# Optimization experiments

Measured on AMD Instinct MI355X. Metric: run time of the kernel, lower is better.

The kernel has to match this reference:

```python
import jax, jax.numpy as jnp
import numpy as np

B, S, D, H = 64, 256, 2048, 16
HD = D // H  # 128
MAXS = 256


def setup_inputs() -> dict:
    key = jax.random.key(0)
    ks = jax.random.split(key, 16)
    sc = 0.02
    inp = {
        "q": jax.random.normal(ks[0], (B, S, D), jnp.float32),
        "k": jax.random.normal(ks[1], (B, S, D), jnp.float32),
        "v": jax.random.normal(ks[2], (B, S, D), jnp.float32),
        "attention_mask": jax.random.randint(ks[3], (B, S), 0, 2, jnp.int32),
        # projection weights, torch Linear convention: y = x @ W.T + b
        "Wq": jax.random.normal(ks[4], (D, D), jnp.float32) * sc,
        "bq": jnp.zeros((D,), jnp.float32),
        "Wk": jax.random.normal(ks[5], (D, D), jnp.float32) * sc,
        "bk": jnp.zeros((D,), jnp.float32),
        "Wv": jax.random.normal(ks[6], (D, D), jnp.float32) * sc,
        "bv": jnp.zeros((D,), jnp.float32),
        "Wo": jax.random.normal(ks[7], (D, D), jnp.float32) * sc,
        "bo": jnp.zeros((D,), jnp.float32),
        # additive per-head bias table (max_sequence_length=256)
        "bias_table": jax.random.normal(ks[8], (H, MAXS, MAXS), jnp.float32) * 0.1,
    }
    return inp


def reference(q, k, v, attention_mask, Wq, bq, Wk, bk, Wv, bv, Wo, bo, bias_table):
    def proj(x, W, b):  # (B,S,D) -> (B,H,S,HD)
        y = x @ W.T + b
        return y.reshape(B, S, H, HD).transpose(0, 2, 1, 3)

    qh = proj(q, Wq, bq)
    kh = proj(k, Wk, bk)
    vh = proj(v, Wv, bv)

    # (B,H,Sq,Sk) scores
    scores = jnp.einsum("bhqd,bhkd->bhqk", qh, kh) / jnp.sqrt(jnp.float32(HD))
    scores = scores + bias_table[None, :, :S, :S]
    # mask: (B,Sk) -> (B,1,1,Sk); masked_fill where mask==0
    neg_inf = jnp.finfo(scores.dtype).min
    scores = jnp.where(attention_mask[:, None, None, :] == 0, neg_inf, scores)
    probs = jax.nn.softmax(scores, axis=-1)  # dropout p=0.0 -> identity
    out = jnp.einsum("bhqk,bhkd->bhqd", probs, vh)
    out = out.transpose(0, 2, 1, 3).reshape(B, S, D)
    return out @ Wo.T + bo
```

## Files before the change

### kernel.cpp

```cpp
#include <hip/hip_runtime.h>
#include <hip/hip_bf16.h>

typedef __attribute__((ext_vector_type(4))) float f32x4;
typedef __attribute__((ext_vector_type(8))) short s16x8;
typedef __attribute__((ext_vector_type(4))) unsigned short u16x4;
typedef __attribute__((ext_vector_type(8))) unsigned short u16x8;
typedef __attribute__((ext_vector_type(4))) int i32x4;

#define NB 64
#define NS 256
#define ND 2048
#define NH 16
#define NHD 128

__device__ __forceinline__ unsigned short f2bf(float f){
  unsigned int u = __float_as_uint(f);
  u += 0x7fffu + ((u >> 16) & 1u);
  return (unsigned short)(u >> 16);
}

__device__ __forceinline__ void gload16(const void* g, void* l){
  __builtin_amdgcn_global_load_lds(
    (const __attribute__((address_space(1))) unsigned int*)g,
    (__attribute__((address_space(3))) unsigned int*)l, 16, 0, 0);
}

#define SBAR()  __builtin_amdgcn_sched_barrier(0)
#define BARRIER() do{ SBAR(); __builtin_amdgcn_s_barrier(); SBAR(); }while(0)
#define WAIT_LGKM0() do{ asm volatile("s_waitcnt lgkmcnt(0)" ::: "memory"); SBAR(); }while(0)
#define WAIT_VM0()   do{ asm volatile("s_waitcnt vmcnt(0)"   ::: "memory"); SBAR(); }while(0)
#define WAIT_VM8()   do{ asm volatile("s_waitcnt vmcnt(8)"   ::: "memory"); SBAR(); }while(0)

__global__ __launch_bounds__(256) void wconv(const float* __restrict__ s,
                                             unsigned short* __restrict__ d, int n8){
  int i = blockIdx.x*256 + threadIdx.x;
  if (i >= n8) return;
  f32x4 a = *(const f32x4*)(s + (size_t)i*8);
  f32x4 b = *(const f32x4*)(s + (size_t)i*8 + 4);
  u16x8 u;
  #pragma unroll
  for (int r=0;r<4;r++){ u[r]=f2bf(a[r]); u[4+r]=f2bf(b[r]); }
  *(u16x8*)(d + (size_t)i*8) = u;
}

template<int OUTMODE>
__global__ __launch_bounds__(512, 2) void gemm256(
    const unsigned short* __restrict__ A, const unsigned short* __restrict__ Bw,
    const float* __restrict__ bias, void* __restrict__ Out, int m_base)
{
  extern __shared__ __attribute__((aligned(16))) char ldsb[];
  const int tid  = threadIdx.x;
  const int lane = tid & 63, wid = tid >> 6;
  const int g = lane >> 4, l15 = lane & 15;
  const int wm = wid >> 2, wn = wid & 3;

  const int nwg = gridDim.x, bid = blockIdx.x;
  const int swz = (bid & 7) * (nwg >> 3) + (bid >> 3);
  const int mt = swz >> 3, nt = swz & 7;
  const int m0 = mt*256, n0 = nt*256;

  const int srow_l = tid >> 3;
  const int scol   = (((tid & 7) ^ (srow_l & 7)) * 8);
  const unsigned short* gsrc[4];
  gsrc[0] = A  + (size_t)(m0 +       srow_l)*ND + scol;
  gsrc[1] = A  + (size_t)(m0 + 128 + srow_l)*ND + scol;
  gsrc[2] = Bw + (size_t)(n0 +       srow_l)*ND + scol;
  gsrc[3] = Bw + (size_t)(n0 + 128 + srow_l)*ND + scol;

#define STAGE(buf, p, kt) do{ \
    const unsigned short* s_ = gsrc[p] + (kt); \
    char* d_ = ldsb + (buf)*65536 + ((p)>>1)*32768 + ((p)&1)*16384 + tid*16; \
    gload16(s_, d_); gload16(s_ + (size_t)64*ND, d_ + 8192); }while(0)

#define RD_A(buf, qa) do{ \
    _Pragma("unroll") for (int i_=0;i_<4;i_++){ \
      int hr = (qa)*64 + i_*16 + l15; \
      const char* p_ = ldsb + (buf)*65536 + wm*16384 + hr*128; \
      _Pragma("unroll") for (int ks_=0;ks_<2;ks_++) \
        av[i_][ks_] = *(const s16x8*)(p_ + (((ks_*4+g) ^ (hr&7))*16)); } }while(0)

#define RD_B(buf, dst, qb) do{ \
    _Pragma("unroll") for (int j_=0;j_<2;j_++){ \
      int hc = (wn&1)*64 + (qb)*32 + j_*16 + l15; \
      const char* p_ = ldsb + (buf)*65536 + 32768 + (wn>>1)*16384 + hc*128; \
      _Pragma("unroll") for (int ks_=0;ks_<2;ks_++) \
        dst[j_][ks_] = *(const s16x8*)(p_ + (((ks_*4+g) ^ (hc&7))*16)); } }while(0)

#define MFMA_PH(qa, qb, bv) do{ \
    __builtin_amdgcn_s_setprio(1); \
    _Pragma("unroll") for (int i_=0;i_<4;i_++) \
      _Pragma("unroll") for (int j_=0;j_<2;j_++) \
        _Pragma("unroll") for (int ks_=0;ks_<2;ks_++) \
          acc[(qa)*4+i_][(qb)*2+j_] = __builtin_amdgcn_mfma_f32_16x16x32_bf16( \
              av[i_][ks_], bv[j_][ks_], acc[(qa)*4+i_][(qb)*2+j_], 0,0,0); \
    __builtin_amdgcn_s_setprio(0); }while(0)

  f32x4 acc[8][4];
  s16x8 av[4][2], bva[2][2], bvb[2][2];

  STAGE(0,0,0); STAGE(0,1,0); STAGE(0,2,0); STAGE(0,3,0);
  #pragma unroll
  for (int i=0;i<8;i++)
    #pragma unroll
    for (int j=0;j<4;j++) acc[i][j] = f32x4{0.f,0.f,0.f,0.f};
  WAIT_VM0();
  BARRIER();

  for (int t = 0; t < 16; ++t) {
    const int kt1 = t*128 + 64, kt2 = t*128 + 128;
    RD_A(0,0); RD_B(0,bva,0);
    STAGE(1,0,kt1); STAGE(1,1,kt1); STAGE(1,2,kt1); STAGE(1,3,kt1);
    BARRIER(); WAIT_LGKM0();
    MFMA_PH(0,0,bva);
    BARRIER();
    RD_B(0,bvb,1);
    BARRIER(); WAIT_LGKM0();
    MFMA_PH(0,1,bvb);
    BARRIER();
    RD_A(0,1);
    BARRIER(); WAIT_LGKM0();
    MFMA_PH(1,0,bva);
    MFMA_PH(1,1,bvb);
    WAIT_VM0();
    BARRIER();
    RD_A(1,0); RD_B(1,bva,0);
    if (t < 15){ STAGE(0,0,kt2); STAGE(0,1,kt2); STAGE(0,2,kt2); STAGE(0,3,kt2); }
    BARRIER(); WAIT_LGKM0();
    MFMA_PH(0,0,bva);
    BARRIER();
    RD_B(1,bvb,1);
    BARRIER(); WAIT_LGKM0();
    MFMA_PH(0,1,bvb);
    BARRIER();
    RD_A(1,1);
    BARRIER(); WAIT_LGKM0();
    MFMA_PH(1,0,bva);
    MFMA_PH(1,1,bvb);
    WAIT_VM0();
    BARRIER();
  }

  #pragma unroll
  for (int jx=0;jx<4;jx++){
    int n = n0 + wn*64 + ((jx>>1)<<5) + ((jx&1)<<4) + l15;
    float bj = bias[n];
    #pragma unroll
    for (int i=0;i<8;i++){
      int mb = m_base + m0 + wm*128 + ((i>>2)<<6) + ((i&3)<<4) + g*4;
      if (OUTMODE == 2){
        float* O = (float*)Out;
        #pragma unroll
        for (int r=0;r<4;r++) O[(size_t)(mb+r)*ND + n] = acc[i][jx][r] + bj;
      } else if (OUTMODE == 0){
        unsigned short* O = (unsigned short*)Out;
        int bb = mb >> 8, h = n >> 7, d = n & 127, s0 = mb & 255;
        #pragma unroll
        for (int r=0;r<4;r++)
          O[(((size_t)bb*NH + h)*NS + s0 + r)*NHD + d] = f2bf(acc[i][jx][r] + bj);
      } else {
        unsigned short* O = (unsigned short*)Out;
        int bb = mb >> 8, h = n >> 7, d = n & 127, s0 = mb & 255;
        u16x4 u;
        #pragma unroll
        for (int r=0;r<4;r++) u[r] = f2bf(acc[i][jx][r] + bj);
        *(u16x4*)(O + (((size_t)bb*NH + h)*NHD + d)*NS + s0) = u;
      }
    }
  }
#undef STAGE
#undef RD_A
#undef RD_B
#undef MFMA_PH
}

__global__ __launch_bounds__(512, 1) void attn_fused2(
  const unsigned short* __restrict__ Qh, const unsigned short* __restrict__ Kh,
  const unsigned short* __restrict__ VT, const int* __restrict__ mask,
  const float* __restrict__ bias_table, unsigned short* __restrict__ AO)
{
  __shared__ unsigned short Klds[256*128];
  __shared__ unsigned short Vlds[128*256];
  char* Kb_ = (char*)Klds; char* Vb_ = (char*)Vlds;
  const int bh = blockIdx.x, b = bh >> 4, h = bh & 15;
  const int tid = threadIdx.x, lane = tid & 63, w = tid >> 6;
  const int g = lane >> 4, l15 = lane & 15;

  {
    const unsigned short* Ksrc = Kh + (size_t)bh*NS*NHD;
    int r0 = tid >> 4, sl = tid & 15;
    #pragma unroll
    for (int c=0;c<8;c++){
      int row = c*32 + r0;
      gload16(Ksrc + (size_t)row*NHD + ((sl ^ (row&7))*8), Kb_ + c*8192 + tid*16);
    }
  }
  {
    const unsigned short* Vsrc = VT + (size_t)bh*NHD*NS;
    int r0 = tid >> 5, sl = tid & 31;
    #pragma unroll
    for (int c=0;c<8;c++){
      int row = c*16 + r0;
      gload16(Vsrc + (size_t)row*NS + ((sl ^ (row&7))*8), Vb_ + c*8192 + tid*16);
    }
  }
  WAIT_VM8();
  BARRIER();

  const float scale = 0.08838834764831845f;
  const int* mrow = mask + b*NS;
  const int s0l = l15 + ((g&1)<<5), s1l = s0l + 16;
  const int sel = g >> 1;

  auto pass = [&](int p, bool wait_v){
    const int q = w*32 + p*16 + l15;
    const unsigned short* Qrow = Qh + ((size_t)bh*NS + q)*NHD;
    s16x8 bq[4];
    #pragma unroll
    for (int kk=0;kk<4;kk++) bq[kk] = *(const s16x8*)(Qrow + kk*32 + g*8);

    f32x4 c[16];
    __builtin_amdgcn_s_setprio(1);
    #pragma unroll
    for (int kb=0;kb<16;kb++){
      c[kb] = f32x4{0.f,0.f,0.f,0.f};
      int row = kb*16 + l15;
      #pragma unroll
      for (int kk=0;kk<4;kk++){
        s16x8 a = *(const s16x8*)(Kb_ + row*256 + (((kk*4+g) ^ (row&7))*16));
        c[kb] = __builtin_amdgcn_mfma_f32_16x16x32_bf16(a, bq[kk], c[kb], 0,0,0);
      }
    }
    __builtin_amdgcn_s_setprio(0);

    const float* brow = bias_table + ((size_t)h*NS + q)*NS;
    float mx = -3.0e38f;
    #pragma unroll
    for (int kb=0;kb<16;kb++){
      f32x4 b4 = *(const f32x4*)(brow + kb*16 + g*4);
      i32x4 m4 = *(const i32x4*)(mrow + kb*16 + g*4);
      #pragma unroll
      for (int r=0;r<4;r++){
        float val = (m4[r] != 0) ? (c[kb][r]*scale + b4[r]) : -3.0e38f;
        c[kb][r] = val;
        mx = fmaxf(mx, val);
      }
    }
    mx = fmaxf(mx, __shfl_xor(mx, 16));
    mx = fmaxf(mx, __shfl_xor(mx, 32));
    float sum = 0.f;
    #pragma unroll
    for (int kb=0;kb<16;kb++)
      #pragma unroll
      for (int r=0;r<4;r++){
        float pv = __expf(c[kb][r] - mx);
        c[kb][r] = pv; sum += pv;
      }
    sum += __shfl_xor(sum, 16);
    sum += __shfl_xor(sum, 32);
    float inv = 1.f / sum;

    unsigned int pk[16][2];
    #pragma unroll
    for (int kb=0;kb<16;kb++){
      pk[kb][0] = (unsigned int)f2bf(c[kb][0]*inv) | ((unsigned int)f2bf(c[kb][1]*inv) << 16);
      pk[kb][1] = (unsigned int)f2bf(c[kb][2]*inv) | ((unsigned int)f2bf(c[kb][3]*inv) << 16);
    }

    if (wait_v){ WAIT_VM0(); BARRIER(); }

    s16x8 pb[8];
    #pragma unroll
    for (int kk=0;kk<8;kk++){
      unsigned int e0 = (unsigned int)__shfl((int)pk[2*kk][0],   s0l);
      unsigned int e1 = (unsigned int)__shfl((int)pk[2*kk][1],   s0l);
      unsigned int e2 = (unsigned int)__shfl((int)pk[2*kk][0],   s1l);
      unsigned int e3 = (unsigned int)__shfl((int)pk[2*kk][1],   s1l);
      unsigned int o0 = (unsigned int)__shfl((int)pk[2*kk+1][0], s0l);
      unsigned int o1 = (unsigned int)__shfl((int)pk[2*kk+1][1], s0l);
      unsigned int o2 = (unsigned int)__shfl((int)pk[2*kk+1][0], s1l);
      unsigned int o3 = (unsigned int)__shfl((int)pk[2*kk+1][1], s1l);
      union { unsigned int wd[4]; s16x8 v; } u_;
      u_.wd[0] = sel ? o0 : e0; u_.wd[1] = sel ? o1 : e1;
      u_.wd[2] = sel ? o2 : e2; u_.wd[3] = sel ? o3 : e3;
      pb[kk] = u_.v;
    }

    f32x4 oacc[8];
    __builtin_amdgcn_s_setprio(1);
    #pragma unroll
    for (int dt=0;dt<8;dt++){
      oacc[dt] = f32x4{0.f,0.f,0.f,0.f};
      int row = dt*16 + l15;
      #pragma unroll
      for (int kk=0;kk<8;kk++){
        s16x8 a = *(const s16x8*)(Vb_ + row*512 + (((kk*4+g) ^ (row&7))*16));
        oacc[dt] = __builtin_amdgcn_mfma_f32_16x16x32_bf16(a, pb[kk], oacc[dt], 0,0,0);
      }
    }
    __builtin_amdgcn_s_setprio(0);

    #pragma unroll
    for (int dt=0;dt<8;dt++){
      u16x4 u;
      #pragma unroll
      for (int r=0;r<4;r++) u[r] = f2bf(oacc[dt][r]);
      *(u16x4*)(AO + ((size_t)b*NS + q)*ND + h*NHD + dt*16 + g*4) = u;
    }
  };

  pass(0, true);
  pass(1, false);
}

extern "C" void kernel_launch(void* const* d_in, const int* in_sizes, int n_in,
                              void* d_out, int out_size, void* d_ws, size_t ws_size,
                              hipStream_t stream)
{
  const float* q  = (const float*)d_in[0];
  const float* k  = (const float*)d_in[1];
  const float* v  = (const float*)d_in[2];
  const int* mask = (const int*)d_in[3];
  const float* Wq = (const float*)d_in[4];
  const float* bq = (const float*)d_in[5];
  const float* Wk = (const float*)d_in[6];
  const float* bk = (const float*)d_in[7];
  const float* Wv = (const float*)d_in[8];
  const float* bv = (const float*)d_in[9];
  const float* Wo = (const float*)d_in[10];
  const float* bo = (const float*)d_in[11];
  const float* bias_table = (const float*)d_in[12];

  char* ws = (char*)d_ws;
  unsigned short* Wob = (unsigned short*)(ws + 0);
  unsigned short* wb  = (unsigned short*)(ws + 8388608);
  unsigned short* tmp = (unsigned short*)(ws + 16777216);
  unsigned short* Qh  = (unsigned short*)(ws + 83886080);
  unsigned short* Kh  = (unsigned short*)(ws + 150994944);
  unsigned short* VT  = (unsigned short*)(ws + 218103808);
  unsigned short* AO  = (unsigned short*)(ws + 285212672);

  hipFuncSetAttribute((const void*)gemm256<0>, hipFuncAttributeMaxDynamicSharedMemorySize, 131072);
  hipFuncSetAttribute((const void*)gemm256<1>, hipFuncAttributeMaxDynamicSharedMemorySize, 131072);
  hipFuncSetAttribute((const void*)gemm256<2>, hipFuncAttributeMaxDynamicSharedMemorySize, 131072);

  wconv<<<2048,256,0,stream>>>(Wo, Wob, 524288);

  const float* acts[3]  = {q, k, v};
  const float* wgt[3]   = {Wq, Wk, Wv};
  const float* bia[3]   = {bq, bk, bv};
  unsigned short* outs[3] = {Qh, Kh, VT};

  for (int x = 0; x < 3; ++x) {
    wconv<<<2048,256,0,stream>>>(wgt[x], wb, 524288);
    wconv<<<16384,256,0,stream>>>(acts[x], tmp, 4194304);
    if (x < 2)
      gemm256<0><<<512,512,131072,stream>>>(tmp, wb, bia[x], outs[x], 0);
    else
      gemm256<1><<<512,512,131072,stream>>>(tmp, wb, bia[x], outs[x], 0);
  }

  attn_fused2<<<1024,512,0,stream>>>(Qh,Kh,VT,mask,bias_table,AO);
  gemm256<2><<<512,512,131072,stream>>>(AO,Wob,bo,(float*)d_out,0);
}
```

Measured before the change: 795.9 us.

## Deepen GEMM pipeline so global loads stay in flight across halves

Reorganizes the projection GEMM main loop so both LDS buffers are prefetched up front. Each half-step now issues the next tile's global-to-LDS loads into the buffer it just finished reading, right before its last MFMA phase. It then waits with a partial vmcnt (8) instead of draining all loads, so one tile's loads overlap the next half's compute. The intent is to hide global memory latency behind MFMA work. The cost is more outstanding loads and correctness that depends on the vmcnt accounting and barrier placement.

```diff
diff --git a/kernel.cpp b/kernel.cpp
--- a/kernel.cpp
+++ b/kernel.cpp
@@ -95,50 +95,43 @@
               av[i_][ks_], bv[j_][ks_], acc[(qa)*4+i_][(qb)*2+j_], 0,0,0); \
     __builtin_amdgcn_s_setprio(0); }while(0)
 
+#define HALF(buf, kt_next, doStage) do{ \
+    RD_A(buf,0); RD_B(buf,bva,0); \
+    BARRIER(); WAIT_LGKM0(); \
+    MFMA_PH(0,0,bva); \
+    BARRIER(); \
+    RD_B(buf,bvb,1); \
+    BARRIER(); WAIT_LGKM0(); \
+    MFMA_PH(0,1,bvb); \
+    BARRIER(); \
+    RD_A(buf,1); \
+    WAIT_LGKM0(); BARRIER(); \
+    if ((doStage)==1){ STAGE(buf,0,kt_next); STAGE(buf,1,kt_next); \
+                       STAGE(buf,2,kt_next); STAGE(buf,3,kt_next); } \
+    MFMA_PH(1,0,bva); \
+    MFMA_PH(1,1,bvb); \
+    if ((doStage)==1){ WAIT_VM8(); BARRIER(); } \
+    else if ((doStage)==2){ WAIT_VM0(); BARRIER(); } \
+  }while(0)
+
   f32x4 acc[8][4];
   s16x8 av[4][2], bva[2][2], bvb[2][2];
 
   STAGE(0,0,0); STAGE(0,1,0); STAGE(0,2,0); STAGE(0,3,0);
+  STAGE(1,0,64); STAGE(1,1,64); STAGE(1,2,64); STAGE(1,3,64);
   #pragma unroll
   for (int i=0;i<8;i++)
     #pragma unroll
     for (int j=0;j<4;j++) acc[i][j] = f32x4{0.f,0.f,0.f,0.f};
-  WAIT_VM0();
+  WAIT_VM8();
   BARRIER();
 
-  for (int t = 0; t < 16; ++t) {
-    const int kt1 = t*128 + 64, kt2 = t*128 + 128;
-    RD_A(0,0); RD_B(0,bva,0);
-    STAGE(1,0,kt1); STAGE(1,1,kt1); STAGE(1,2,kt1); STAGE(1,3,kt1);
-    BARRIER(); WAIT_LGKM0();
-    MFMA_PH(0,0,bva);
-    BARRIER();
-    RD_B(0,bvb,1);
-    BARRIER(); WAIT_LGKM0();
-    MFMA_PH(0,1,bvb);
-    BARRIER();
-    RD_A(0,1);
-    BARRIER(); WAIT_LGKM0();
-    MFMA_PH(1,0,bva);
-    MFMA_PH(1,1,bvb);
-    WAIT_VM0();
-    BARRIER();
-    RD_A(1,0); RD_B(1,bva,0);
-    if (t < 15){ STAGE(0,0,kt2); STAGE(0,1,kt2); STAGE(0,2,kt2); STAGE(0,3,kt2); }
-    BARRIER(); WAIT_LGKM0();
-    MFMA_PH(0,0,bva);
-    BARRIER();
-    RD_B(1,bvb,1);
-    BARRIER(); WAIT_LGKM0();
-    MFMA_PH(0,1,bvb);
-    BARRIER();
-    RD_A(1,1);
-    BARRIER(); WAIT_LGKM0();
-    MFMA_PH(1,0,bva);
-    MFMA_PH(1,1,bvb);
-    WAIT_VM0();
-    BARRIER();
-  }
+  for (int t = 0; t < 15; ++t) {
+    HALF(0, (2*t+2)*64, 1);
+    HALF(1, (2*t+3)*64, 1);
+  }
+  HALF(0, 0, 2);
+  HALF(1, 0, 3);
 
   #pragma unroll
   for (int jx=0;jx<4;jx++){
@@ -171,6 +164,7 @@
 #undef RD_A
 #undef RD_B
 #undef MFMA_PH
+#undef HALF
 }
 
 __global__ __launch_bounds__(512, 1) void attn_fused2(
```

Measured after the change: 778.3 us. 1.02x faster.
